# Performance work log

Hardware: AMD Instinct MI355X
Metric: run time of the kernel (lower is better)

## Reference

```python
import jax, jax.numpy as jnp
import numpy as np

NUM_CITIES = 128
NUM_ATTRS = 128
NUM_HIDDENS = 512
BATCH = 1024


def setup_inputs() -> dict:
    key = jax.random.key(0)
    ks = jax.random.split(key, 8)
    inp = {
        "input": jax.random.normal(ks[0], (BATCH, NUM_CITIES, NUM_ATTRS), dtype=jnp.float32),
        "state": jax.random.normal(ks[1], (BATCH, NUM_CITIES, NUM_HIDDENS), dtype=jnp.float32),
        "w_z": jax.random.normal(ks[2], (NUM_ATTRS, NUM_HIDDENS), dtype=jnp.float32) / 100.0,
        "u_z": jax.random.normal(ks[3], (NUM_HIDDENS, NUM_HIDDENS), dtype=jnp.float32) / 100.0,
        "b_z": jnp.zeros((NUM_HIDDENS,), dtype=jnp.float32),
        "w_r": jax.random.normal(ks[4], (NUM_ATTRS, NUM_HIDDENS), dtype=jnp.float32) / 100.0,
        "u_r": jax.random.normal(ks[5], (NUM_HIDDENS, NUM_HIDDENS), dtype=jnp.float32) / 100.0,
        "b_r": jnp.zeros((NUM_HIDDENS,), dtype=jnp.float32),
        "w_h": jax.random.normal(ks[6], (NUM_ATTRS, NUM_HIDDENS), dtype=jnp.float32) / 100.0,
        "u_h": jax.random.normal(ks[7], (NUM_HIDDENS, NUM_HIDDENS), dtype=jnp.float32) / 100.0,
        "b_h": jnp.zeros((NUM_HIDDENS,), dtype=jnp.float32),
    }
    return inp


def reference(input, state, w_z, u_z, b_z, w_r, u_r, b_r, w_h, u_h, b_h):
    # Flatten (batch, cities) into row dim, as the torch module does.
    x = input.reshape(-1, NUM_ATTRS)          # [B*C, A]
    h = state.reshape(-1, NUM_HIDDENS)        # [B*C, H]
    z = jax.nn.sigmoid(x @ w_z + h @ u_z + b_z)
    r = jax.nn.sigmoid(x @ w_r + h @ u_r + b_r)
    h_tilde = jnp.tanh(x @ w_h + (r * h) @ u_h + b_h)
    h_new = (1.0 - z) * h + z * h_tilde
    return h_new.reshape(-1, NUM_CITIES, NUM_HIDDENS)
```

## Files before the change

### kernel.cpp

```cpp
#include <hip/hip_runtime.h>
#include <cstdint>
#include <cstddef>


#define M_ROWS 131072
#define A_DIM 128
#define H_DIM 512
#define K_TOT 640
#define BK 32
#define NSTEPS 20
#define XSTEPS 4
#define BM 256
#define BN 128
#define SLOT_B 24576

typedef _Float16 f16;
typedef _Float16 f16x8 __attribute__((ext_vector_type(8)));
typedef float f32x4 __attribute__((ext_vector_type(4)));

#define AS1 __attribute__((address_space(1)))
#define AS3 __attribute__((address_space(3)))

__device__ __forceinline__ void gload_lds16(const void* g, void* l) {
  __builtin_amdgcn_global_load_lds((const AS1 unsigned int*)g,
                                   (AS3 unsigned int*)l, 16, 0, 0);
}

__device__ __forceinline__ float sigmoid_f(float v) {
  return __builtin_amdgcn_rcpf(1.0f + __expf(-v));
}
__device__ __forceinline__ float tanh_f(float v) {
  float c = fminf(fmaxf(v, -15.0f), 15.0f);
  float e = __expf(2.0f * c);
  return (e - 1.0f) * __builtin_amdgcn_rcpf(e + 1.0f);
}


__global__ void build_wcat(const float* __restrict__ wz, const float* __restrict__ uz,
                           const float* __restrict__ wr, const float* __restrict__ ur,
                           const float* __restrict__ wh, const float* __restrict__ uh,
                           f16* __restrict__ B1, f16* __restrict__ B2) {
  int idx = blockIdx.x * blockDim.x + threadIdx.x;
  const int n1 = 1024 * K_TOT;
  if (idx < n1) {
    int n = idx / K_TOT, k = idx % K_TOT;
    float v;
    if (k < A_DIM) v = (n < H_DIM) ? wz[k * H_DIM + n] : wr[k * H_DIM + (n - H_DIM)];
    else           v = (n < H_DIM) ? uz[(k - A_DIM) * H_DIM + n] : ur[(k - A_DIM) * H_DIM + (n - H_DIM)];
    B1[idx] = (f16)v;
  } else {
    int idx2 = idx - n1;
    if (idx2 < H_DIM * K_TOT) {
      int n = idx2 / K_TOT, k = idx2 % K_TOT;
      float v = (k < A_DIM) ? wh[k * H_DIM + n] : uh[(k - A_DIM) * H_DIM + n];
      B2[idx2] = (f16)v;
    }
  }
}

__global__ void cvt2_f32_f16(const float* __restrict__ a, long na,
                             const float* __restrict__ b, long nb,
                             f16* __restrict__ a16, f16* __restrict__ b16) {
  long i = (long)blockIdx.x * blockDim.x + threadIdx.x;
  const long stride = (long)gridDim.x * blockDim.x;
  const long tot = (na + nb) >> 3;
  for (; i < tot; i += stride) {
    const float* src; f16* dst; long e;
    if (i * 8 < na) { src = a; dst = a16; e = i * 8; }
    else            { src = b; dst = b16; e = i * 8 - na; }
    float4 v0 = *(const float4*)(src + e);
    float4 v1 = *(const float4*)(src + e + 4);
    f16x8 o;
    o[0] = (_Float16)v0.x; o[1] = (_Float16)v0.y; o[2] = (_Float16)v0.z; o[3] = (_Float16)v0.w;
    o[4] = (_Float16)v1.x; o[5] = (_Float16)v1.y; o[6] = (_Float16)v1.z; o[7] = (_Float16)v1.w;
    *(f16x8*)(dst + e) = o;
  }
}

template <int MODE>
__global__ __launch_bounds__(512, 4)
void gru_gemm16p(const f16* __restrict__ A0, const f16* __restrict__ A1,
                 const f16* __restrict__ h16, const f16* __restrict__ Bt,
                 const float* __restrict__ bias0, const float* __restrict__ bias1,
                 float* __restrict__ out, f16* __restrict__ rh_out,
                 f16* __restrict__ z16) {
  constexpr int NBLK = (MODE == 1) ? 8 : 4;
  __shared__ __align__(16) char smem[3 * SLOT_B];

  const int per = gridDim.x >> 3;
  const int b = blockIdx.x;
  const int tile = (b & 7) * per + (b >> 3);
  const int nb = tile & (NBLK - 1);
  const int mb = tile / NBLK;
  const int m0 = mb * BM;
  const int n0 = nb * BN;

  const int tid = threadIdx.x;
  const int lane = tid & 63;
  const int wid = tid >> 6;
  const int wm = wid >> 1;
  const int wn = wid & 1;
  const int r16 = lane & 15;
  const int kh = lane >> 4;

  f32x4 acc[4][4];
#pragma unroll
  for (int i = 0; i < 4; ++i)
#pragma unroll
    for (int j = 0; j < 4; ++j) acc[i][j] = (f32x4){0.f, 0.f, 0.f, 0.f};

  auto dma_A = [&](int t, int slot) {
    char* Aw = smem + slot * SLOT_B;
    const f16* src = (t < XSTEPS) ? A0 : A1;
    const int ld = (t < XSTEPS) ? A_DIM : H_DIM;
    const int colb = (t < XSTEPS) ? t * BK : t * BK - A_DIM;
#pragma unroll
    for (int j = 0; j < 2; ++j) {
      const int s = j * 512 + tid;
      const int row = s >> 2;
      const int c = (s & 3) ^ ((row >> 1) & 3);
      const f16* g = src + (size_t)(m0 + row) * ld + colb + c * 8;
      gload_lds16(g, Aw + j * 8192 + wid * 1024);
    }
  };
  auto dma_B = [&](int t, int slot) {
    char* Bw = smem + slot * SLOT_B + 16384;
    const int s = tid;
    const int row = s >> 2;
    const int c = (s & 3) ^ ((row >> 1) & 3);
    const f16* g = Bt + (size_t)(n0 + row) * K_TOT + t * BK + c * 8;
    gload_lds16(g, Bw + wid * 1024);
  };

  dma_A(0, 0); dma_B(0, 0);
  dma_A(1, 1); dma_B(1, 1);

  int aoff[4], boff[4];
#pragma unroll
  for (int mi = 0; mi < 4; ++mi) {
    const int ra = wm * 64 + mi * 16 + r16;
    aoff[mi] = ra * 64 + ((kh ^ ((ra >> 1) & 3)) << 4);
  }
#pragma unroll
  for (int ni = 0; ni < 4; ++ni) {
    const int rb = wn * 64 + ni * 16 + r16;
    boff[ni] = 16384 + rb * 64 + ((kh ^ ((rb >> 1) & 3)) << 4);
  }

  for (int t = 0; t < NSTEPS; ++t) {
    if (t < NSTEPS - 1) asm volatile("s_waitcnt vmcnt(3)" ::: "memory");
    else                asm volatile("s_waitcnt vmcnt(0)" ::: "memory");
    __builtin_amdgcn_s_barrier();
    asm volatile("" ::: "memory");

    const char* Sl = smem + (t % 3) * SLOT_B;
    f16x8 aF[4], bF[4];
#pragma unroll
    for (int mi = 0; mi < 4; ++mi) aF[mi] = *(const f16x8*)(Sl + aoff[mi]);
#pragma unroll
    for (int ni = 0; ni < 4; ++ni) bF[ni] = *(const f16x8*)(Sl + boff[ni]);

    if (t + 2 < NSTEPS) {
      dma_A(t + 2, (t + 2) % 3);
      dma_B(t + 2, (t + 2) % 3);
    }

    asm volatile("s_waitcnt lgkmcnt(0)" ::: "memory");
    __builtin_amdgcn_s_setprio(1);
#pragma unroll
    for (int mi = 0; mi < 4; ++mi)
#pragma unroll
      for (int ni = 0; ni < 4; ++ni)
        acc[mi][ni] = __builtin_amdgcn_mfma_f32_16x16x32_f16(aF[mi], bF[ni], acc[mi][ni], 0, 0, 0);
    __builtin_amdgcn_s_setprio(0);
    asm volatile("" ::: "memory");
    __builtin_amdgcn_s_barrier();
    asm volatile("" ::: "memory");
  }

  const bool zhalf = (MODE == 1) && (n0 < H_DIM);
  float b4[4];
#pragma unroll
  for (int ni = 0; ni < 4; ++ni) {
    const int n_g = n0 + wn * 64 + ni * 16 + r16;
    b4[ni] = (MODE == 2) ? bias0[n_g] : (zhalf ? bias0[n_g] : bias1[n_g - H_DIM]);
  }
  __syncthreads();
  char* ep = smem;
#pragma unroll
  for (int mi = 0; mi < 4; ++mi) {
#pragma unroll
    for (int ni = 0; ni < 4; ++ni) {
      const int C = wn * 64 + ni * 16 + r16;
      const int sw = ((C >> 3) ^ (kh << 1)) << 4;
      const int cb = (C & 7) * 2;
#pragma unroll
      for (int r = 0; r < 4; ++r) {
        const int R = wm * 64 + mi * 16 + kh * 4 + r;
        const float v = acc[mi][ni][r] + b4[ni];
        const float a = (MODE == 2) ? tanh_f(v) : sigmoid_f(v);
        *(f16*)(ep + R * 256 + sw + cb) = (f16)a;
      }
    }
  }
  __syncthreads();

#pragma unroll
  for (int j = 0; j < 8; ++j) {
    const int sIdx = j * 512 + tid;
    const int R = sIdx >> 4;
    const int ss = sIdx & 15;
    const int sr = ss ^ (((R >> 2) & 3) << 1);
    const f16x8 tv = *(const f16x8*)(ep + R * 256 + sr * 16);
    const size_t m_g = (size_t)(m0 + R);
    if (MODE == 1) {
      if (zhalf) {
        const size_t off = m_g * H_DIM + n0 + ss * 8;
        if (z16) {
          *(f16x8*)(z16 + off) = tv;
        } else {
          float4 o0, o1;
          o0.x = (float)tv[0]; o0.y = (float)tv[1]; o0.z = (float)tv[2]; o0.w = (float)tv[3];
          o1.x = (float)tv[4]; o1.y = (float)tv[5]; o1.z = (float)tv[6]; o1.w = (float)tv[7];
          *(float4*)(out + off) = o0;
          *(float4*)(out + off + 4) = o1;
        }
      } else {
        const size_t off = m_g * H_DIM + (n0 - H_DIM) + ss * 8;
        const f16x8 hv = *(const f16x8*)(h16 + off);
        f16x8 rv;
#pragma unroll
        for (int e = 0; e < 8; ++e) rv[e] = (f16)((float)tv[e] * (float)hv[e]);
        *(f16x8*)(rh_out + off) = rv;
      }
    } else {
      const size_t off = m_g * H_DIM + n0 + ss * 8;
      const f16x8 hv = *(const f16x8*)(h16 + off);
      float zz[8];
      if (z16) {
        const f16x8 zv = *(const f16x8*)(z16 + off);
#pragma unroll
        for (int e = 0; e < 8; ++e) zz[e] = (float)zv[e];
      } else {
        const float4 z0 = *(const float4*)(out + off);
        const float4 z1 = *(const float4*)(out + off + 4);
        zz[0] = z0.x; zz[1] = z0.y; zz[2] = z0.z; zz[3] = z0.w;
        zz[4] = z1.x; zz[5] = z1.y; zz[6] = z1.z; zz[7] = z1.w;
      }
      float4 o0, o1;
      float oo[8];
#pragma unroll
      for (int e = 0; e < 8; ++e) {
        const float hh = (float)hv[e];
        oo[e] = fmaf(zz[e], (float)tv[e] - hh, hh);
      }
      o0.x = oo[0]; o0.y = oo[1]; o0.z = oo[2]; o0.w = oo[3];
      o1.x = oo[4]; o1.y = oo[5]; o1.z = oo[6]; o1.w = oo[7];
      *(float4*)(out + off) = o0;
      *(float4*)(out + off + 4) = o1;
    }
  }
}

template <int MODE>
__global__ __launch_bounds__(256, 2)
void gru_gemm_fb(const float* __restrict__ x, const float* __restrict__ h,
                 const f16* __restrict__ Bt, const f16* __restrict__ rh_in,
                 const float* __restrict__ bias0, const float* __restrict__ bias1,
                 float* __restrict__ out, f16* __restrict__ rh_out) {
  constexpr int NBLK = (MODE == 1) ? 8 : 4;
  __shared__ __align__(16) char smem[2 * 16384];

  const int per = gridDim.x >> 3;
  const int b = blockIdx.x;
  const int tile = (b & 7) * per + (b >> 3);
  const int nb = tile & (NBLK - 1);
  const int mb = tile / NBLK;
  const int m0 = mb * 128;
  const int n0 = nb * 128;

  const int tid = threadIdx.x;
  const int lane = tid & 63;
  const int wid = tid >> 6;
  const int wm = wid >> 1;
  const int wn = wid & 1;
  const int r16 = lane & 15;
  const int kh = lane >> 4;

  f32x4 acc[4][4];
#pragma unroll
  for (int i = 0; i < 4; ++i)
#pragma unroll
    for (int j = 0; j < 4; ++j) acc[i][j] = (f32x4){0.f, 0.f, 0.f, 0.f};

  float4 fa0, fa1, fa2, fa3;

  auto dma_B = [&](int t, int buf) {
    char* Bw = smem + buf * 16384 + 8192;
#pragma unroll
    for (int i = 0; i < 2; ++i) {
      const int chunk = wid * 2 + i;
      const int s = chunk * 64 + lane;
      const int row = s >> 2, c = s & 3;
      const f16* g = Bt + (size_t)(n0 + row) * K_TOT + t * BK + c * 8;
      gload_lds16(g, Bw + chunk * 1024);
    }
  };
  auto dma_A_rh = [&](int t, int buf) {
    char* Aw = smem + buf * 16384;
    const int col = t * BK - A_DIM;
#pragma unroll
    for (int i = 0; i < 2; ++i) {
      const int chunk = wid * 2 + i;
      const int s = chunk * 64 + lane;
      const int row = s >> 2, c = s & 3;
      const f16* g = rh_in + (size_t)(m0 + row) * H_DIM + col + c * 8;
      gload_lds16(g, Aw + chunk * 1024);
    }
  };
  auto load_A_regs = [&](int t) {
    const float* src = (t < XSTEPS) ? x : h;
    const int ld = (t < XSTEPS) ? A_DIM : H_DIM;
    const int col = (t < XSTEPS) ? t * BK : t * BK - A_DIM;
    {
      const int s = tid, row = s >> 2, c = s & 3;
      const float* g = src + (size_t)(m0 + row) * ld + col + c * 8;
      fa0 = *(const float4*)g;
      fa1 = *(const float4*)(g + 4);
    }
    {
      const int s = tid + 256, row = s >> 2, c = s & 3;
      const float* g = src + (size_t)(m0 + row) * ld + col + c * 8;
      fa2 = *(const float4*)g;
      fa3 = *(const float4*)(g + 4);
    }
  };
  auto write_A = [&](int buf) {
    char* Aw = smem + buf * 16384;
    f16x8 v;
    v[0] = (_Float16)fa0.x; v[1] = (_Float16)fa0.y; v[2] = (_Float16)fa0.z; v[3] = (_Float16)fa0.w;
    v[4] = (_Float16)fa1.x; v[5] = (_Float16)fa1.y; v[6] = (_Float16)fa1.z; v[7] = (_Float16)fa1.w;
    *(f16x8*)(Aw + tid * 16) = v;
    f16x8 w;
    w[0] = (_Float16)fa2.x; w[1] = (_Float16)fa2.y; w[2] = (_Float16)fa2.z; w[3] = (_Float16)fa2.w;
    w[4] = (_Float16)fa3.x; w[5] = (_Float16)fa3.y; w[6] = (_Float16)fa3.z; w[7] = (_Float16)fa3.w;
    *(f16x8*)(Aw + (tid + 256) * 16) = w;
  };

  dma_B(0, 0);
  load_A_regs(0);
  write_A(0);
  __syncthreads();

  int cur = 0;
  for (int t = 0; t < NSTEPS; ++t) {
    const int nxt = t + 1;
    const bool have = nxt < NSTEPS;
    const bool nxt_dma_A = (MODE == 2) && (nxt >= XSTEPS);
    if (have) {
      dma_B(nxt, cur ^ 1);
      if (nxt_dma_A) dma_A_rh(nxt, cur ^ 1);
      else load_A_regs(nxt);
    }
    const char* Al = smem + cur * 16384;
    const char* Bl = Al + 8192;
    f16x8 aF[4], bF[4];
#pragma unroll
    for (int mi = 0; mi < 4; ++mi)
      aF[mi] = *(const f16x8*)(Al + (wm * 64 + mi * 16 + r16) * 64 + kh * 16);
#pragma unroll
    for (int ni = 0; ni < 4; ++ni)
      bF[ni] = *(const f16x8*)(Bl + (wn * 64 + ni * 16 + r16) * 64 + kh * 16);
#pragma unroll
    for (int mi = 0; mi < 4; ++mi)
#pragma unroll
      for (int ni = 0; ni < 4; ++ni)
        acc[mi][ni] = __builtin_amdgcn_mfma_f32_16x16x32_f16(aF[mi], bF[ni], acc[mi][ni], 0, 0, 0);
    if (have && !nxt_dma_A) write_A(cur ^ 1);
    __syncthreads();
    cur ^= 1;
  }

#pragma unroll
  for (int mi = 0; mi < 4; ++mi) {
#pragma unroll
    for (int ni = 0; ni < 4; ++ni) {
      const int n_g = n0 + wn * 64 + ni * 16 + r16;
#pragma unroll
      for (int r = 0; r < 4; ++r) {
        const int m_g = m0 + wm * 64 + mi * 16 + kh * 4 + r;
        float v = acc[mi][ni][r];
        if (MODE == 1) {
          if (n_g < H_DIM) {
            out[(size_t)m_g * H_DIM + n_g] = sigmoid_f(v + bias0[n_g]);
          } else {
            const int j = n_g - H_DIM;
            const size_t off = (size_t)m_g * H_DIM + j;
            float rv = sigmoid_f(v + bias1[j]);
            rh_out[off] = (f16)(rv * h[off]);
          }
        } else {
          const size_t off = (size_t)m_g * H_DIM + n_g;
          float th = tanh_f(v + bias0[n_g]);
          float zv = out[off];
          float hv = h[off];
          out[off] = fmaf(zv, th - hv, hv);
        }
      }
    }
  }
}

extern "C" void kernel_launch(void* const* d_in, const int* in_sizes, int n_in,
                              void* d_out, int out_size, void* d_ws, size_t ws_size,
                              hipStream_t stream) {
  const float* x  = (const float*)d_in[0];
  const float* h  = (const float*)d_in[1];
  const float* wz = (const float*)d_in[2];
  const float* uz = (const float*)d_in[3];
  const float* bz = (const float*)d_in[4];
  const float* wr = (const float*)d_in[5];
  const float* ur = (const float*)d_in[6];
  const float* br = (const float*)d_in[7];
  const float* wh = (const float*)d_in[8];
  const float* uh = (const float*)d_in[9];
  const float* bh = (const float*)d_in[10];
  float* out = (float*)d_out;

  char* ws = (char*)d_ws;
  const size_t B1_B  = (size_t)1024 * K_TOT * 2;
  const size_t B2_B  = (size_t)H_DIM * K_TOT * 2;
  const size_t RH_B  = (size_t)M_ROWS * H_DIM * 2;
  const size_t X16_B = (size_t)M_ROWS * A_DIM * 2;
  const size_t H16_B = RH_B;
  const size_t Z16_B = RH_B;

  f16* B1 = (f16*)ws;
  f16* B2 = (f16*)(ws + B1_B);
  f16* rh = (f16*)(ws + B1_B + B2_B);

  const size_t need_base = B1_B + B2_B + RH_B + X16_B + H16_B;
  const int wtot = 1024 * K_TOT + H_DIM * K_TOT;

  if (ws_size >= need_base) {
    f16* x16 = (f16*)(ws + B1_B + B2_B + RH_B);
    f16* h16 = (f16*)(ws + B1_B + B2_B + RH_B + X16_B);
    f16* z16 = (ws_size >= need_base + Z16_B) ? (f16*)(ws + need_base) : nullptr;

    build_wcat<<<dim3((wtot + 255) / 256), dim3(256), 0, stream>>>(wz, uz, wr, ur, wh, uh, B1, B2);
    cvt2_f32_f16<<<dim3(4096), dim3(256), 0, stream>>>(
        x, (long)M_ROWS * A_DIM, h, (long)M_ROWS * H_DIM, x16, h16);
    gru_gemm16p<1><<<dim3((M_ROWS / BM) * 8), dim3(512), 0, stream>>>(
        x16, h16, h16, B1, bz, br, out, rh, z16);
    gru_gemm16p<2><<<dim3((M_ROWS / BM) * 4), dim3(512), 0, stream>>>(
        x16, rh, h16, B2, bh, nullptr, out, nullptr, z16);
  } else {
    build_wcat<<<dim3((wtot + 255) / 256), dim3(256), 0, stream>>>(wz, uz, wr, ur, wh, uh, B1, B2);
    gru_gemm_fb<1><<<dim3((M_ROWS / 128) * 8), dim3(256), 0, stream>>>(x, h, B1, nullptr, bz, br, out, rh);
    gru_gemm_fb<2><<<dim3((M_ROWS / 128) * 4), dim3(256), 0, stream>>>(x, h, B2, rh, bh, nullptr, out, rh);
  }
}
```

Measured before the change: 571.6 us.

## Deepen GEMM pipeline to four LDS stages with register double-buffered fragments

Moves the fused GRU GEMM kernels from a 3-slot to a 4-slot LDS ring with three tiles in flight. Fragments are double-buffered in registers, so LDS reads for step t+1 are issued before the MFMAs for step t run. One of the two barriers per k-step is removed. The costs are more LDS and registers, and launch bounds drop from 4 to 2 blocks per CU, which lowers occupancy.

```diff
diff --git a/kernel.cpp b/kernel.cpp
--- a/kernel.cpp
+++ b/kernel.cpp
@@ -78,14 +78,14 @@
 }
 
 template <int MODE>
-__global__ __launch_bounds__(512, 4)
-void gru_gemm16p(const f16* __restrict__ A0, const f16* __restrict__ A1,
+__global__ __launch_bounds__(512, 2)
+void gru_gemm16q(const f16* __restrict__ A0, const f16* __restrict__ A1,
                  const f16* __restrict__ h16, const f16* __restrict__ Bt,
                  const float* __restrict__ bias0, const float* __restrict__ bias1,
                  float* __restrict__ out, f16* __restrict__ rh_out,
                  f16* __restrict__ z16) {
   constexpr int NBLK = (MODE == 1) ? 8 : 4;
-  __shared__ __align__(16) char smem[3 * SLOT_B];
+  __shared__ __align__(16) char smem[4 * SLOT_B];
 
   const int per = gridDim.x >> 3;
   const int b = blockIdx.x;
@@ -132,9 +132,6 @@
     gload_lds16(g, Bw + wid * 1024);
   };
 
-  dma_A(0, 0); dma_B(0, 0);
-  dma_A(1, 1); dma_B(1, 1);
-
   int aoff[4], boff[4];
 #pragma unroll
   for (int mi = 0; mi < 4; ++mi) {
@@ -147,25 +144,16 @@
     boff[ni] = 16384 + rb * 64 + ((kh ^ ((rb >> 1) & 3)) << 4);
   }
 
-  for (int t = 0; t < NSTEPS; ++t) {
-    if (t < NSTEPS - 1) asm volatile("s_waitcnt vmcnt(3)" ::: "memory");
-    else                asm volatile("s_waitcnt vmcnt(0)" ::: "memory");
-    __builtin_amdgcn_s_barrier();
-    asm volatile("" ::: "memory");
-
-    const char* Sl = smem + (t % 3) * SLOT_B;
-    f16x8 aF[4], bF[4];
+  f16x8 aX[4], bX[4], aY[4], bY[4];
+
+  auto dsread = [&](int t, f16x8* aF, f16x8* bF) {
+    const char* Sl = smem + (t & 3) * SLOT_B;
 #pragma unroll
     for (int mi = 0; mi < 4; ++mi) aF[mi] = *(const f16x8*)(Sl + aoff[mi]);
 #pragma unroll
     for (int ni = 0; ni < 4; ++ni) bF[ni] = *(const f16x8*)(Sl + boff[ni]);
-
-    if (t + 2 < NSTEPS) {
-      dma_A(t + 2, (t + 2) % 3);
-      dma_B(t + 2, (t + 2) % 3);
-    }
-
-    asm volatile("s_waitcnt lgkmcnt(0)" ::: "memory");
+  };
+  auto mfma16 = [&](const f16x8* aF, const f16x8* bF) {
     __builtin_amdgcn_s_setprio(1);
 #pragma unroll
     for (int mi = 0; mi < 4; ++mi)
@@ -173,10 +161,37 @@
       for (int ni = 0; ni < 4; ++ni)
         acc[mi][ni] = __builtin_amdgcn_mfma_f32_16x16x32_f16(aF[mi], bF[ni], acc[mi][ni], 0, 0, 0);
     __builtin_amdgcn_s_setprio(0);
-    asm volatile("" ::: "memory");
+  };
+
+  dma_A(0, 0); dma_B(0, 0);
+  dma_A(1, 1); dma_B(1, 1);
+  dma_A(2, 2); dma_B(2, 2);
+  asm volatile("s_waitcnt vmcnt(6)" ::: "memory");
+  __builtin_amdgcn_s_barrier();
+  dsread(0, aX, bX);
+
+  auto body = [&](int t, f16x8* aC, f16x8* bC, f16x8* aN, f16x8* bN) {
+    if (t < NSTEPS - 2) asm volatile("s_waitcnt vmcnt(3)" ::: "memory");
+    else                asm volatile("s_waitcnt vmcnt(0)" ::: "memory");
     __builtin_amdgcn_s_barrier();
-    asm volatile("" ::: "memory");
-  }
+    dsread(t + 1, aN, bN);
+    if (t + 3 < NSTEPS) {
+      dma_A(t + 3, (t + 3) & 3);
+      dma_B(t + 3, (t + 3) & 3);
+    }
+    asm volatile("s_waitcnt lgkmcnt(8)" ::: "memory");
+    __builtin_amdgcn_sched_barrier(0);
+    mfma16(aC, bC);
+  };
+
+  for (int t = 0; t < NSTEPS - 2; t += 2) {
+    body(t,     aX, bX, aY, bY);
+    body(t + 1, aY, bY, aX, bX);
+  }
+  body(NSTEPS - 2, aX, bX, aY, bY);
+  asm volatile("s_waitcnt lgkmcnt(0)" ::: "memory");
+  __builtin_amdgcn_sched_barrier(0);
+  mfma16(aY, bY);
 
   const bool zhalf = (MODE == 1) && (n0 < H_DIM);
   float b4[4];
@@ -450,9 +465,9 @@
     build_wcat<<<dim3((wtot + 255) / 256), dim3(256), 0, stream>>>(wz, uz, wr, ur, wh, uh, B1, B2);
     cvt2_f32_f16<<<dim3(4096), dim3(256), 0, stream>>>(
         x, (long)M_ROWS * A_DIM, h, (long)M_ROWS * H_DIM, x16, h16);
-    gru_gemm16p<1><<<dim3((M_ROWS / BM) * 8), dim3(512), 0, stream>>>(
+    gru_gemm16q<1><<<dim3((M_ROWS / BM) * 8), dim3(512), 0, stream>>>(
         x16, h16, h16, B1, bz, br, out, rh, z16);
-    gru_gemm16p<2><<<dim3((M_ROWS / BM) * 4), dim3(512), 0, stream>>>(
+    gru_gemm16q<2><<<dim3((M_ROWS / BM) * 4), dim3(512), 0, stream>>>(
         x16, rh, h16, B2, bh, nullptr, out, nullptr, z16);
   } else {
     build_wcat<<<dim3((wtot + 255) / 256), dim3(256), 0, stream>>>(wz, uz, wr, ur, wh, uh, B1, B2);
```

Result: slower. 663.0 us (+16.0%).
